# Optimization experiments

Measured on AMD Instinct MI355X. Metric: run time of the kernel, lower is better.

Reference implementation:

```python
import jax, jax.numpy as jnp
import numpy as np

K = 3            # char conv window (in words of chars)
B, P, LC = 64, 80, 18   # batch, padded sentence len, padded word char len
E = 256          # embedding_dim (shared by word and char embeddings)
H = 1024         # lstm hidden
L_CH = 4         # conv output channels
VOCAB, ALPHA, TAGS = 50000, 100, 50


def setup_inputs() -> dict:
    key = jax.random.key(0)
    ks = jax.random.split(key, 12)
    D = E + L_CH  # lstm input dim
    s = 0.02
    return {
        "sentence_batch": jax.random.randint(ks[0], (B, P), 0, VOCAB),
        "character_batch": jax.random.randint(ks[1], (B, P, LC), 0, ALPHA),
        "word_emb": jax.random.normal(ks[2], (VOCAB, E), jnp.float32) * s,
        "char_emb": jax.random.normal(ks[3], (ALPHA, E), jnp.float32) * s,
        "conv_w": jax.random.normal(ks[4], (L_CH, K * E), jnp.float32) * s,
        "conv_b": jax.random.normal(ks[5], (L_CH,), jnp.float32) * s,
        "w_ih": jax.random.normal(ks[6], (4 * H, D), jnp.float32) * s,
        "w_hh": jax.random.normal(ks[7], (4 * H, H), jnp.float32) * s,
        "b_ih": jax.random.normal(ks[8], (4 * H,), jnp.float32) * s,
        "b_hh": jax.random.normal(ks[9], (4 * H,), jnp.float32) * s,
        "out_w": jax.random.normal(ks[10], (TAGS, H), jnp.float32) * s,
        "out_b": jax.random.normal(ks[11], (TAGS,), jnp.float32) * s,
    }


def reference(sentence_batch, character_batch, word_emb, char_emb, conv_w,
              conv_b, w_ih, w_hh, b_ih, b_hh, out_w, out_b):
    # --- char CNN: sliding K-window over char embeddings, flatten, linear, max ---
    ce = char_emb[character_batch]                      # [B,P,LC,E]
    Wn = LC - K + 1                                     # windows per word
    widx = jnp.arange(Wn)[:, None] + jnp.arange(K)      # [Wn,K]
    win = ce[:, :, widx, :].reshape(B, P, Wn, K * E)    # [B,P,Wn,K*E]
    # Conv1d(in=1, out=4, kernel=K*E) on a length-K*E input == one linear per window
    phi = jnp.einsum('bpwd,cd->bpwc', win, conv_w) + conv_b  # [B,P,Wn,4]
    char_repr = phi.max(axis=2)                         # [B,P,4] (max over windows)

    # --- word embeddings + concat ---
    we = word_emb[sentence_batch]                       # [B,P,E]
    combined = jnp.concatenate([we, char_repr], axis=2) # [B,P,E+4]
    D = combined.shape[-1]
    # faithful to torch: .view(PADDING_SIZE, BATCH_SIZE, -1) is a reshape, not transpose
    x = combined.reshape(P, B, D)                       # [P,B,D]

    # --- LSTM (torch gate order i,f,g,o) ---
    def step(carry, x_t):
        h, c = carry
        gates = x_t @ w_ih.T + b_ih + h @ w_hh.T + b_hh  # [B,4H]
        i, f, g, o = jnp.split(gates, 4, axis=-1)
        i = jax.nn.sigmoid(i)
        f = jax.nn.sigmoid(f)
        g = jnp.tanh(g)
        o = jax.nn.sigmoid(o)
        c = f * c + i * g
        h = o * jnp.tanh(c)
        return (h, c), h

    h0 = jnp.zeros((B, H), x.dtype)
    c0 = jnp.zeros((B, H), x.dtype)
    _, hs = jax.lax.scan(step, (h0, c0), x)             # [P,B,H]

    # faithful reshape back, linear head, log_softmax over dim=1 (the P axis)
    lstm_out = hs.reshape(B, P, H)
    tag_space = lstm_out @ out_w.T + out_b              # [B,P,TAGS]
    return jax.nn.log_softmax(tag_space, axis=1)
```

## Files before the change

### kernel.cpp

```cpp
#include <hip/hip_runtime.h>
#include <math.h>

#define BB 64
#define PP 80
#define LC 18
#define EE 256
#define HH 1024
#define LCH 4
#define KW 3
#define TAGS 50
#define DD 260
#define KPAD 288
#define ROWS (BB*PP)
#define WN (LC-KW+1)
#define NG (4*HH)
#define GRP 4
#define UPB 32
#define NBLK (GRP*(HH/UPB))
#define HSTEP32 (GRP*32*512)

typedef __attribute__((ext_vector_type(8))) short short8;
typedef __attribute__((ext_vector_type(4))) short short4v;
typedef __attribute__((ext_vector_type(4))) float floatx4;
typedef __attribute__((ext_vector_type(4))) int int4v;

__device__ __forceinline__ short f2bf(float x) {
    unsigned u = __float_as_uint(x);
    unsigned r = (u + 0x7FFFu + ((u >> 16) & 1u)) >> 16;
    return (short)r;
}
__device__ __forceinline__ float bf2f(short s) {
    return __uint_as_float(((unsigned)(unsigned short)s) << 16);
}
__device__ __forceinline__ float sigf(float x) { return 1.f / (1.f + __expf(-x)); }
__device__ __forceinline__ float tanhfast(float x) {
    float e = __expf(2.f * x);
    return 1.f - 2.f / (e + 1.f);
}
__device__ __forceinline__ float wave_reduce_sum(float v) {
    for (int off = 32; off > 0; off >>= 1) v += __shfl_xor(v, off, 64);
    return v;
}

__global__ __launch_bounds__(256) void prep_kernel(
    const float* __restrict__ wih, const float* __restrict__ whh,
    const float* __restrict__ outw,
    short* __restrict__ wih_bf, short* __restrict__ wpk,
    short* __restrict__ outw_bf, unsigned* __restrict__ hst32)
{
    const int NI = NG * KPAD;
    const int NH = NG * HH;
    const int NO = 64 * HH;
    const int total = NI + NH + NO;
    for (int i = blockIdx.x * 256 + threadIdx.x; i < total; i += gridDim.x * 256) {
        if (i < NI) {
            int r = i / KPAD, c = i - r * KPAD;
            wih_bf[i] = (c < DD) ? f2bf(wih[r * DD + c]) : (short)0;
        } else if (i < NI + NH) {
            int o = i - NI;
            int e  = o & 7;
            int l  = (o >> 3) & 63;
            int s  = (o >> 9) & 3;
            int tl = (o >> 11) & 7;
            int w  = (o >> 14) & 7;
            int bl = o >> 17;
            int row = (tl >> 1) * HH + bl * 32 + (tl & 1) * 16 + (l & 15);
            int col = w * 128 + s * 32 + (l >> 4) * 8 + e;
            wpk[o] = f2bf(whh[(size_t)row * HH + col]);
        } else {
            int k = i - NI - NH;
            int r = k >> 10;
            outw_bf[k] = (r < TAGS) ? f2bf(outw[k]) : (short)0;
        }
    }
    int4v z = {0, 0, 0, 0};
    int4v* hz = (int4v*)hst32;
    const int NZ = PP * HSTEP32 / 4;
    for (int i = blockIdx.x * 256 + threadIdx.x; i < NZ; i += gridDim.x * 256)
        hz[i] = z;
}

__global__ __launch_bounds__(256) void embed_kernel(
    const int* __restrict__ sent, const int* __restrict__ chars,
    const float* __restrict__ word_emb, const float* __restrict__ char_emb,
    const float* __restrict__ conv_w, const float* __restrict__ conv_b,
    short* __restrict__ X)
{
    __shared__ float4 ce[LC * 64];
    __shared__ float phi[WN * LCH];
    __shared__ float charrep[LCH];
    const int r = blockIdx.x;
    const int t = threadIdx.x;
    const int lane = t & 63, wv = t >> 6;

    const int cbase = r * LC;
    for (int i = 0; i < 5; ++i) {
        int idx = i * 256 + t;
        if (idx < LC * 64) {
            int j = idx >> 6, e4 = idx & 63;
            int ch = chars[cbase + j];
            ce[idx] = ((const float4*)(char_emb + (size_t)ch * EE))[e4];
        }
    }
    float4 cw[KW][LCH];
    #pragma unroll
    for (int k = 0; k < KW; ++k)
        #pragma unroll
        for (int c = 0; c < LCH; ++c)
            cw[k][c] = ((const float4*)(conv_w + c * (KW * EE) + k * EE))[lane];
    __syncthreads();

    #pragma unroll
    for (int wi = 0; wi < 4; ++wi) {
        int w = wv + wi * 4;
        float acc[LCH] = {0.f, 0.f, 0.f, 0.f};
        #pragma unroll
        for (int k = 0; k < KW; ++k) {
            float4 v = ce[(w + k) * 64 + lane];
            #pragma unroll
            for (int c = 0; c < LCH; ++c)
                acc[c] += v.x * cw[k][c].x + v.y * cw[k][c].y +
                          v.z * cw[k][c].z + v.w * cw[k][c].w;
        }
        #pragma unroll
        for (int c = 0; c < LCH; ++c) {
            float s = wave_reduce_sum(acc[c]);
            if (lane == 0) phi[w * LCH + c] = s;
        }
    }
    __syncthreads();
    if (t < LCH) {
        float m = -1e30f;
        for (int w = 0; w < WN; ++w) m = fmaxf(m, phi[w * LCH + t]);
        charrep[t] = m + conv_b[t];
    }
    __syncthreads();

    const int word = sent[r];
    X[(size_t)r * KPAD + t] = f2bf(word_emb[(size_t)word * EE + t]);
    if (t < LCH) X[(size_t)r * KPAD + EE + t] = f2bf(charrep[t]);
    if (t >= 228) X[(size_t)r * KPAD + 32 + t] = (short)0;
}

__global__ __launch_bounds__(256) void gemm_in_kernel(
    const short* __restrict__ X, const short* __restrict__ Wih,
    const float* __restrict__ b_ih, const float* __restrict__ b_hh,
    short* __restrict__ ginP)
{
    const int tid = threadIdx.x;
    const int l = tid & 63, wv = tid >> 6;
    const int r0 = blockIdx.x * 64;
    const int n0 = blockIdx.y * 128 + wv * 32;
    const int lr = l & 15, lh = l >> 4;

    floatx4 acc[4][2];
    #pragma unroll
    for (int m = 0; m < 4; ++m)
        #pragma unroll
        for (int n = 0; n < 2; ++n) acc[m][n] = (floatx4)0.f;

    const short* Xb = X + (size_t)(r0 + lr) * KPAD + lh * 8;
    const short* Wb = Wih + (size_t)(n0 + lr) * KPAD + lh * 8;

    #pragma unroll
    for (int k0 = 0; k0 < KPAD; k0 += 32) {
        short8 a0 = *(const short8*)(Xb + k0);
        short8 a1 = *(const short8*)(Xb + 16 * KPAD + k0);
        short8 a2 = *(const short8*)(Xb + 32 * KPAD + k0);
        short8 a3 = *(const short8*)(Xb + 48 * KPAD + k0);
        short8 b0 = *(const short8*)(Wb + k0);
        short8 b1 = *(const short8*)(Wb + 16 * KPAD + k0);
        acc[0][0] = __builtin_amdgcn_mfma_f32_16x16x32_bf16(a0, b0, acc[0][0], 0, 0, 0);
        acc[1][0] = __builtin_amdgcn_mfma_f32_16x16x32_bf16(a1, b0, acc[1][0], 0, 0, 0);
        acc[2][0] = __builtin_amdgcn_mfma_f32_16x16x32_bf16(a2, b0, acc[2][0], 0, 0, 0);
        acc[3][0] = __builtin_amdgcn_mfma_f32_16x16x32_bf16(a3, b0, acc[3][0], 0, 0, 0);
        acc[0][1] = __builtin_amdgcn_mfma_f32_16x16x32_bf16(a0, b1, acc[0][1], 0, 0, 0);
        acc[1][1] = __builtin_amdgcn_mfma_f32_16x16x32_bf16(a1, b1, acc[1][1], 0, 0, 0);
        acc[2][1] = __builtin_amdgcn_mfma_f32_16x16x32_bf16(a2, b1, acc[2][1], 0, 0, 0);
        acc[3][1] = __builtin_amdgcn_mfma_f32_16x16x32_bf16(a3, b1, acc[3][1], 0, 0, 0);
    }
    #pragma unroll
    for (int m = 0; m < 4; ++m)
        #pragma unroll
        for (int n = 0; n < 2; ++n) {
            int col = n0 + n * 16 + lr;
            float bias = b_ih[col] + b_hh[col];
            short4v pack;
            #pragma unroll
            for (int q = 0; q < 4; ++q) pack[q] = f2bf(acc[m][n][q] + bias);
            int w_ = col >> 10, bl_ = (col >> 4) & 63, uu_ = col & 15;
            size_t addr = ((((size_t)(blockIdx.x * GRP + m) * 64 + bl_) * 4 + w_) * 16
                           + uu_) * 16 + lh * 4;
            *(short4v*)(ginP + addr) = pack;
        }
}

__global__ __launch_bounds__(512, 1) void lstm_seq_kernel(
    unsigned* __restrict__ hst, const short* __restrict__ wpk,
    const short* __restrict__ ginP)
{
    __shared__ __align__(16) float lds_g[8][8][16][20];

    const int tid = threadIdx.x;
    const int l = tid & 63;
    const int w = tid >> 6;
    const int g  = blockIdx.x >> 5;
    const int bl = blockIdx.x & 31;

    short8 barr[8][4];
    {
        const short* wb = wpk + (size_t)(bl * 8 + w) * 16384 + l * 8;
        #pragma unroll
        for (int tl = 0; tl < 8; ++tl)
            #pragma unroll
            for (int s = 0; s < 4; ++s)
                barr[tl][s] = *(const short8*)(wb + tl * 2048 + s * 512);
    }

    const int b16 = tid & 15;
    const int uu  = tid >> 4;
    const int U_  = bl * 32 + uu;
    float c = 0.f;

    const size_t hoff = (size_t)g * 16384 + bl * 512
                        + ((uu >> 3) * 16 + b16) * 8 + (uu & 7);

    float gv[4];
    {
        const short* gb = ginP + (((size_t)g * 64 + (U_ >> 4)) * 4) * 256
                          + (U_ & 15) * 16 + b16;
        #pragma unroll
        for (int q = 0; q < 4; ++q) gv[q] = bf2f(gb[q * 256]);
    }

    for (int t = 0; t < PP; ++t) {
        if (t > 0) {
            const unsigned* A = hst + (size_t)(t - 1) * HSTEP32 + g * 16384
                                + (w * 4) * 512 + l * 8;
            int4v d[8];
            unsigned stale = 0xFu;
            do {
                #pragma unroll
                for (int s = 0; s < 4; ++s)
                    if (stale & (1u << s)) {
                        asm volatile("global_load_dwordx4 %0, %1, off sc0 sc1"
                                     : "=v"(d[2 * s]) : "v"(A + s * 512) : "memory");
                        asm volatile("global_load_dwordx4 %0, %1, off sc0 sc1"
                                     : "=v"(d[2 * s + 1]) : "v"(A + s * 512 + 4) : "memory");
                    }
                asm volatile("s_waitcnt vmcnt(0)" ::: "memory");
                __builtin_amdgcn_sched_barrier(0);
                #pragma unroll
                for (int s = 0; s < 4; ++s)
                    if (stale & (1u << s)) {
                        int ok = 1;
                        #pragma unroll
                        for (int i = 0; i < 2; ++i)
                            #pragma unroll
                            for (int j = 0; j < 4; ++j)
                                ok &= ((((unsigned)d[2 * s + i][j]) & 0xFFFFu)
                                       == (unsigned)t);
                        if (__all(ok)) stale &= ~(1u << s);
                    }
                if (stale) __builtin_amdgcn_s_sleep(1);
            } while (stale);

            floatx4 acc[8];
            #pragma unroll
            for (int tl = 0; tl < 8; ++tl) acc[tl] = (floatx4)0.f;
            #pragma unroll
            for (int s = 0; s < 4; ++s) {
                int4v pk;
                pk[0] = (int)((((unsigned)d[2*s][0]) >> 16)   | (((unsigned)d[2*s][1])   & 0xFFFF0000u));
                pk[1] = (int)((((unsigned)d[2*s][2]) >> 16)   | (((unsigned)d[2*s][3])   & 0xFFFF0000u));
                pk[2] = (int)((((unsigned)d[2*s+1][0]) >> 16) | (((unsigned)d[2*s+1][1]) & 0xFFFF0000u));
                pk[3] = (int)((((unsigned)d[2*s+1][2]) >> 16) | (((unsigned)d[2*s+1][3]) & 0xFFFF0000u));
                short8 av = __builtin_bit_cast(short8, pk);
                #pragma unroll
                for (int tl = 0; tl < 8; ++tl)
                    acc[tl] = __builtin_amdgcn_mfma_f32_16x16x32_bf16(
                        av, barr[tl][s], acc[tl], 0, 0, 0);
            }
            #pragma unroll
            for (int tl = 0; tl < 8; ++tl)
                *(floatx4*)&lds_g[w][tl][l & 15][(l >> 4) * 4] = acc[tl];
            __syncthreads();
        }

        {
            float s0 = gv[0], s1 = gv[1], s2 = gv[2], s3 = gv[3];
            if (t > 0) {
                #pragma unroll
                for (int w2 = 0; w2 < 8; ++w2) {
                    s0 += lds_g[w2][0 + (uu >> 4)][uu & 15][b16];
                    s1 += lds_g[w2][2 + (uu >> 4)][uu & 15][b16];
                    s2 += lds_g[w2][4 + (uu >> 4)][uu & 15][b16];
                    s3 += lds_g[w2][6 + (uu >> 4)][uu & 15][b16];
                }
            }
            float i_ = sigf(s0), f_ = sigf(s1), g_ = tanhfast(s2), o_ = sigf(s3);
            c = f_ * c + i_ * g_;
            unsigned hd = (((unsigned)(unsigned short)f2bf(o_ * tanhfast(c))) << 16)
                          | (unsigned)(t + 1);
            unsigned* hp = hst + (size_t)t * HSTEP32 + hoff;
            asm volatile("global_store_dword %0, %1, off sc0 sc1"
                         :: "v"(hp), "v"(hd) : "memory");

            if (t + 1 < PP) {
                const short* gb = ginP + ((((size_t)(t + 1) * GRP + g) * 64
                                          + (U_ >> 4)) * 4) * 256 + (U_ & 15) * 16 + b16;
                #pragma unroll
                for (int q = 0; q < 4; ++q) gv[q] = bf2f(gb[q * 256]);
            }
        }
        __syncthreads();
    }
}

__global__ __launch_bounds__(256) void tagsm_kernel(
    const unsigned* __restrict__ hst, const short* __restrict__ outw_bf,
    const float* __restrict__ out_b, float* __restrict__ out)
{
    __shared__ float sm[PP][52];
    __shared__ float lzb[64];
    const int tid = threadIdx.x;
    const int l = tid & 63, wv = tid >> 6;
    const int b = blockIdx.x;
    const int lr = l & 15, lh = l >> 4;

    const short* Bw = outw_bf + (size_t)(wv * 16 + lr) * HH + lh * 8;

    floatx4 acc[5];
    #pragma unroll
    for (int m = 0; m < 5; ++m) acc[m] = (floatx4)0.f;

    for (int kk = 0; kk < 32; ++kk) {
        short8 bfr = *(const short8*)(Bw + kk * 32);
        #pragma unroll
        for (int m = 0; m < 5; ++m) {
            int q = b * PP + m * 16 + lr;
            int t = q >> 6, gg = (q >> 4) & 3, b16 = q & 15;
            const unsigned* ap = hst + (size_t)t * HSTEP32 + gg * 16384
                                 + kk * 512 + (lh * 16 + b16) * 8;
            int4v d0 = *(const int4v*)(ap);
            int4v d1 = *(const int4v*)(ap + 4);
            int4v pk;
            pk[0] = (int)((((unsigned)d0[0]) >> 16) | (((unsigned)d0[1]) & 0xFFFF0000u));
            pk[1] = (int)((((unsigned)d0[2]) >> 16) | (((unsigned)d0[3]) & 0xFFFF0000u));
            pk[2] = (int)((((unsigned)d1[0]) >> 16) | (((unsigned)d1[1]) & 0xFFFF0000u));
            pk[3] = (int)((((unsigned)d1[2]) >> 16) | (((unsigned)d1[3]) & 0xFFFF0000u));
            short8 a = __builtin_bit_cast(short8, pk);
            acc[m] = __builtin_amdgcn_mfma_f32_16x16x32_bf16(a, bfr, acc[m], 0, 0, 0);
        }
    }
    int col = wv * 16 + lr;
    if (col < TAGS) {
        float bias = out_b[col];
        #pragma unroll
        for (int m = 0; m < 5; ++m)
            #pragma unroll
            for (int q4 = 0; q4 < 4; ++q4)
                sm[m * 16 + lh * 4 + q4][col] = acc[m][q4] + bias;
    }
    __syncthreads();

    if (tid < TAGS) {
        float mx = -1e30f;
        for (int p = 0; p < PP; ++p) mx = fmaxf(mx, sm[p][tid]);
        float s = 0.f;
        for (int p = 0; p < PP; ++p) s += __expf(sm[p][tid] - mx);
        lzb[tid] = mx + __logf(s);
    }
    __syncthreads();

    for (int idx = tid; idx < PP * TAGS; idx += 256) {
        int p = idx / TAGS, j = idx - p * TAGS;
        out[(size_t)b * (PP * TAGS) + idx] = sm[p][j] - lzb[j];
    }
}

extern "C" void kernel_launch(void* const* d_in, const int* in_sizes, int n_in,
                              void* d_out, int out_size, void* d_ws, size_t ws_size,
                              hipStream_t stream)
{
    const int*   sent     = (const int*)d_in[0];
    const int*   chars    = (const int*)d_in[1];
    const float* word_emb = (const float*)d_in[2];
    const float* char_emb = (const float*)d_in[3];
    const float* conv_w   = (const float*)d_in[4];
    const float* conv_b   = (const float*)d_in[5];
    const float* w_ih     = (const float*)d_in[6];
    const float* w_hh     = (const float*)d_in[7];
    const float* b_ih     = (const float*)d_in[8];
    const float* b_hh     = (const float*)d_in[9];
    const float* out_w    = (const float*)d_in[10];
    const float* out_b    = (const float*)d_in[11];
    float* out = (float*)d_out;

    short* X_bf     = (short*)d_ws;
    short* wih_bf   = X_bf + (size_t)ROWS * KPAD;
    short* wpk      = wih_bf + (size_t)NG * KPAD;
    short* outw_bf  = wpk + (size_t)NG * HH;
    short* ginP     = outw_bf + (size_t)64 * HH;
    unsigned* hst32 = (unsigned*)(ginP + (size_t)NG * ROWS);

    hipLaunchKernelGGL(prep_kernel, dim3(2048), dim3(256), 0, stream,
                       w_ih, w_hh, out_w, wih_bf, wpk, outw_bf, hst32);
    hipLaunchKernelGGL(embed_kernel, dim3(ROWS), dim3(256), 0, stream,
                       sent, chars, word_emb, char_emb, conv_w, conv_b, X_bf);
    hipLaunchKernelGGL(gemm_in_kernel, dim3(ROWS / 64, NG / 128), dim3(256), 0, stream,
                       X_bf, wih_bf, b_ih, b_hh, ginP);
    {
        void* kargs[3] = { (void*)&hst32, (void*)&wpk, (void*)&ginP };
        hipLaunchCooperativeKernel((void*)lstm_seq_kernel, dim3(NBLK), dim3(512),
                                   kargs, 0, stream);
    }
    hipLaunchKernelGGL(tagsm_kernel, dim3(BB), dim3(256), 0, stream,
                       hst32, outw_bf, out_b, out);
}
```

Before: 417.3 us.

## Split LSTM batch into 8 groups of 8 and relax cache coherence on polling

The persistent LSTM recurrence now splits the batch into 8 groups of 8 rows instead of 4 groups of 16. Blocks are interleaved so a block's group is the low bits of its index, and the hidden-state exchange buffer and gate-input layouts are rewritten to match. The spin-wait poll first uses loads without the sc1 bit and only falls back to fully coherent loads after several retries. Each h store is also issued a second time without sc1. This halves the work per block and aims to cut sync latency, but half of each MFMA tile is wasted and only 256 of 512 threads do elementwise work. The non-sc1 reads also risk returning stale data on the first polls.

New measurement: 616.0 us. 47.6% more time.

```diff
diff --git a/kernel.cpp b/kernel.cpp
--- a/kernel.cpp
+++ b/kernel.cpp
@@ -14,10 +14,9 @@
 #define ROWS (BB*PP)
 #define WN (LC-KW+1)
 #define NG (4*HH)
-#define GRP 4
-#define UPB 32
-#define NBLK (GRP*(HH/UPB))
-#define HSTEP32 (GRP*32*512)
+#define NGRP 8
+#define NBLK (NGRP*32)
+#define HSTEP32 (NGRP*32*256)
 
 typedef __attribute__((ext_vector_type(8))) short short8;
 typedef __attribute__((ext_vector_type(4))) short short4v;
@@ -188,9 +187,12 @@
             short4v pack;
             #pragma unroll
             for (int q = 0; q < 4; ++q) pack[q] = f2bf(acc[m][n][q] + bias);
-            int w_ = col >> 10, bl_ = (col >> 4) & 63, uu_ = col & 15;
-            size_t addr = ((((size_t)(blockIdx.x * GRP + m) * 64 + bl_) * 4 + w_) * 16
-                           + uu_) * 16 + lh * 4;
+            int gate = col >> 10, u = col & 1023;
+            int bl_ = u >> 5, uu_ = u & 31;
+            int g8 = m * 2 + (lh >> 1);
+            int b8 = (lh & 1) * 4;
+            size_t addr = ((((size_t)(blockIdx.x * NGRP + g8) * 32 + bl_) * 4 + gate)
+                           * 32 + uu_) * 8 + b8;
             *(short4v*)(ginP + addr) = pack;
         }
 }
@@ -199,13 +201,13 @@
     unsigned* __restrict__ hst, const short* __restrict__ wpk,
     const short* __restrict__ ginP)
 {
-    __shared__ __align__(16) float lds_g[8][8][16][20];
+    __shared__ __align__(16) float lds_g[8][8][16][10];
 
     const int tid = threadIdx.x;
     const int l = tid & 63;
     const int w = tid >> 6;
-    const int g  = blockIdx.x >> 5;
-    const int bl = blockIdx.x & 31;
+    const int g  = blockIdx.x & 7;
+    const int bl = blockIdx.x >> 3;
 
     short8 barr[8][4];
     {
@@ -217,37 +219,47 @@
                 barr[tl][s] = *(const short8*)(wb + tl * 2048 + s * 512);
     }
 
-    const int b16 = tid & 15;
-    const int uu  = tid >> 4;
-    const int U_  = bl * 32 + uu;
+    const int uu = tid >> 3;
+    const int b8 = tid & 7;
     float c = 0.f;
 
-    const size_t hoff = (size_t)g * 16384 + bl * 512
-                        + ((uu >> 3) * 16 + b16) * 8 + (uu & 7);
+    const size_t hoff = (size_t)g * 8192 + bl * 256
+                        + ((uu >> 3) * 8 + b8) * 8 + (uu & 7);
 
     float gv[4];
-    {
-        const short* gb = ginP + (((size_t)g * 64 + (U_ >> 4)) * 4) * 256
-                          + (U_ & 15) * 16 + b16;
+    if (tid < 256) {
+        const short* gb = ginP + (((size_t)g * 32 + bl) * 4) * 256 + uu * 8 + b8;
         #pragma unroll
         for (int q = 0; q < 4; ++q) gv[q] = bf2f(gb[q * 256]);
     }
 
     for (int t = 0; t < PP; ++t) {
         if (t > 0) {
-            const unsigned* A = hst + (size_t)(t - 1) * HSTEP32 + g * 16384
-                                + (w * 4) * 512 + l * 8;
+            const unsigned* A = hst + (size_t)(t - 1) * HSTEP32 + g * 8192
+                                + (w * 4) * 256 + ((l >> 4) * 8 + (l & 7)) * 8;
             int4v d[8];
             unsigned stale = 0xFu;
+            int tries = 0;
             do {
-                #pragma unroll
-                for (int s = 0; s < 4; ++s)
-                    if (stale & (1u << s)) {
-                        asm volatile("global_load_dwordx4 %0, %1, off sc0 sc1"
-                                     : "=v"(d[2 * s]) : "v"(A + s * 512) : "memory");
-                        asm volatile("global_load_dwordx4 %0, %1, off sc0 sc1"
-                                     : "=v"(d[2 * s + 1]) : "v"(A + s * 512 + 4) : "memory");
-                    }
+                if (tries < 4) {
+                    #pragma unroll
+                    for (int s = 0; s < 4; ++s)
+                        if (stale & (1u << s)) {
+                            asm volatile("global_load_dwordx4 %0, %1, off sc0"
+                                         : "=v"(d[2 * s]) : "v"(A + s * 256) : "memory");
+                            asm volatile("global_load_dwordx4 %0, %1, off sc0"
+                                         : "=v"(d[2 * s + 1]) : "v"(A + s * 256 + 4) : "memory");
+                        }
+                } else {
+                    #pragma unroll
+                    for (int s = 0; s < 4; ++s)
+                        if (stale & (1u << s)) {
+                            asm volatile("global_load_dwordx4 %0, %1, off sc0 sc1"
+                                         : "=v"(d[2 * s]) : "v"(A + s * 256) : "memory");
+                            asm volatile("global_load_dwordx4 %0, %1, off sc0 sc1"
+                                         : "=v"(d[2 * s + 1]) : "v"(A + s * 256 + 4) : "memory");
+                        }
+                }
                 asm volatile("s_waitcnt vmcnt(0)" ::: "memory");
                 __builtin_amdgcn_sched_barrier(0);
                 #pragma unroll
@@ -262,7 +274,7 @@
                                        == (unsigned)t);
                         if (__all(ok)) stale &= ~(1u << s);
                     }
-                if (stale) __builtin_amdgcn_s_sleep(1);
+                if (stale) { ++tries; __builtin_amdgcn_s_sleep(1); }
             } while (stale);
 
             floatx4 acc[8];
@@ -281,21 +293,25 @@
                     acc[tl] = __builtin_amdgcn_mfma_f32_16x16x32_bf16(
                         av, barr[tl][s], acc[tl], 0, 0, 0);
             }
-            #pragma unroll
-            for (int tl = 0; tl < 8; ++tl)
-                *(floatx4*)&lds_g[w][tl][l & 15][(l >> 4) * 4] = acc[tl];
+            if (l < 32) {
+                #pragma unroll
+                for (int tl = 0; tl < 8; ++tl)
+                    #pragma unroll
+                    for (int q = 0; q < 4; ++q)
+                        lds_g[w][tl][l & 15][(l >> 4) * 4 + q] = acc[tl][q];
+            }
             __syncthreads();
         }
 
-        {
+        if (tid < 256) {
             float s0 = gv[0], s1 = gv[1], s2 = gv[2], s3 = gv[3];
             if (t > 0) {
                 #pragma unroll
                 for (int w2 = 0; w2 < 8; ++w2) {
-                    s0 += lds_g[w2][0 + (uu >> 4)][uu & 15][b16];
-                    s1 += lds_g[w2][2 + (uu >> 4)][uu & 15][b16];
-                    s2 += lds_g[w2][4 + (uu >> 4)][uu & 15][b16];
-                    s3 += lds_g[w2][6 + (uu >> 4)][uu & 15][b16];
+                    s0 += lds_g[w2][0 + (uu >> 4)][uu & 15][b8];
+                    s1 += lds_g[w2][2 + (uu >> 4)][uu & 15][b8];
+                    s2 += lds_g[w2][4 + (uu >> 4)][uu & 15][b8];
+                    s3 += lds_g[w2][6 + (uu >> 4)][uu & 15][b8];
                 }
             }
             float i_ = sigf(s0), f_ = sigf(s1), g_ = tanhfast(s2), o_ = sigf(s3);
@@ -305,10 +321,12 @@
             unsigned* hp = hst + (size_t)t * HSTEP32 + hoff;
             asm volatile("global_store_dword %0, %1, off sc0 sc1"
                          :: "v"(hp), "v"(hd) : "memory");
+            asm volatile("global_store_dword %0, %1, off sc0"
+                         :: "v"(hp), "v"(hd) : "memory");
 
             if (t + 1 < PP) {
-                const short* gb = ginP + ((((size_t)(t + 1) * GRP + g) * 64
-                                          + (U_ >> 4)) * 4) * 256 + (U_ & 15) * 16 + b16;
+                const short* gb = ginP + ((((size_t)(t + 1) * NGRP + g) * 32 + bl) * 4)
+                                  * 256 + uu * 8 + b8;
                 #pragma unroll
                 for (int q = 0; q < 4; ++q) gv[q] = bf2f(gb[q * 256]);
             }
@@ -339,9 +357,10 @@
         #pragma unroll
         for (int m = 0; m < 5; ++m) {
             int q = b * PP + m * 16 + lr;
-            int t = q >> 6, gg = (q >> 4) & 3, b16 = q & 15;
-            const unsigned* ap = hst + (size_t)t * HSTEP32 + gg * 16384
-                                 + kk * 512 + (lh * 16 + b16) * 8;
+            int t = q >> 6, b2 = q & 63;
+            int g8 = b2 >> 3, b8 = b2 & 7;
+            const unsigned* ap = hst + (size_t)t * HSTEP32 + g8 * 8192
+                                 + kk * 256 + (lh * 8 + b8) * 8;
             int4v d0 = *(const int4v*)(ap);
             int4v d1 = *(const int4v*)(ap + 4);
             int4v pk;
```
